# Performance work log

Hardware: AMD Instinct MI355X
Metric: run time of the kernel (lower is better)

## Reference

```python
import jax, jax.numpy as jnp
import numpy as np

B, T, D, R = 4, 2048, 512, 1024
N_INNER, N_B = 9, 2          # inner pool bins, boundary pool bins (roipool_size='2_9')
RATIO = 1.0 / 5.0            # boundary extension ratio passed to BRoI1DPool
NB = N_B + N_INNER + N_B     # 13 total bins: [start bins | inner bins | end bins]


def _bin_centers(a, b, n):
    # a, b: (B, R) -> (B, R, n) centers of n equal bins covering [a, b]
    i = (jnp.arange(n, dtype=a.dtype) + 0.5) / n
    return a[..., None] + i * (b - a)[..., None]


def broi1d_pool(feats, rois):
    # Boundary ROI 1D pooling: feats (B, T, D), rois (B, R, 2) -> (B, R, D, NB).
    # Each bin samples its center position via linear interpolation along T.
    s, e = rois[..., 0], rois[..., 1]
    ext = RATIO * (e - s)
    pos = jnp.concatenate([
        _bin_centers(s - ext, s + ext, N_B),
        _bin_centers(s, e, N_INNER),
        _bin_centers(e - ext, e + ext, N_B)], axis=-1)          # (B, R, NB)
    pos = jnp.clip(pos, 0.0, T - 1)
    lo = jnp.floor(pos).astype(jnp.int32)
    hi = jnp.minimum(lo + 1, T - 1)
    w = (pos - lo.astype(pos.dtype))[..., None]

    def gather(idx):
        g = jnp.take_along_axis(feats, idx.reshape(idx.shape[0], -1)[..., None], axis=1)
        return g.reshape(idx.shape + (feats.shape[-1],))          # (B, R, NB, D)

    vals = (1.0 - w) * gather(lo) + w * gather(hi)
    return vals.transpose(0, 1, 3, 2)                              # (B, R, D, NB)


def setup_inputs():
    key = jax.random.key(0)
    ks = jax.random.split(key, 10)
    features = jax.random.normal(ks[0], (B, T, D), jnp.float32)

    def make_rois(k):
        k1, k2 = jax.random.split(k)
        s = jax.random.uniform(k1, (B, R), jnp.float32, 0.0, T - 300.0)
        L = 16.0 + jax.random.uniform(k2, (B, R), jnp.float32) * 256.0
        return jnp.stack([s, s + L], axis=-1)

    rois = make_rois(ks[1])
    start_rois = make_rois(ks[2])
    end_rois = make_rois(ks[3])
    rois_mask = jnp.ones((B, R), jnp.float32)
    rois_pos_emb = jax.random.normal(ks[4], (B, R, D), jnp.float32)

    d_left = (N_B + N_INNER // 2 + 1) * D
    W_left = jax.random.normal(ks[5], (D, d_left), jnp.float32) / np.sqrt(d_left).astype(np.float32)
    b_left = jnp.zeros((D,), jnp.float32)
    W_inner = jax.random.normal(ks[6], (D, N_INNER * D), jnp.float32) / np.sqrt(N_INNER * D).astype(np.float32)
    b_inner = jnp.zeros((D,), jnp.float32)
    W_roi = jax.random.normal(ks[7], (D, 2 * D), jnp.float32) / np.sqrt(2 * D).astype(np.float32)
    b_roi = jnp.zeros((D,), jnp.float32)
    return {"features": features, "start_rois": start_rois, "end_rois": end_rois,
            "rois": rois, "rois_mask": rois_mask, "rois_pos_emb": rois_pos_emb,
            "W_left": W_left, "b_left": b_left, "W_inner": W_inner, "b_inner": b_inner,
            "W_roi": W_roi, "b_roi": b_roi}


def reference(features, start_rois, end_rois, rois, rois_mask, rois_pos_emb,
              W_left, b_left, W_inner, b_inner, W_roi, b_roi):
    pooled = broi1d_pool(features, rois)          # (B, R, D, NB)
    mb, r = pooled.shape[:2]

    def fc(x, W, b):
        # Linear + Dropout(eval=identity) + SELU
        return jax.nn.selu(x @ W.T + b)

    left = fc(pooled[:, :, :, 0:N_INNER // 2 + N_B + 1].reshape(mb, r, -1), W_left, b_left)
    inner = fc(pooled[:, :, :, N_B:N_INNER + N_B].reshape(mb, r, -1), W_inner, b_inner)
    # NOTE: the original code reuses left_fc for the right branch (right_fc is dead).
    right = fc(pooled[:, :, :, N_INNER // 2 + N_B:N_INNER + 2 * N_B].reshape(mb, r, -1), W_left, b_left)
    return fc(jnp.concatenate([right - left, inner], axis=2), W_roi, b_roi)  # (B, R, D)
```

## Files before the change

kernel.cpp:

```cpp
#include <hip/hip_runtime.h>
#include <hip/hip_bf16.h>
#include <cstdint>
#include <cmath>

#define BB 4
#define TT 2048
#define DD 512
#define RR 1024
#define MM (BB*RR)
#define NBINS 13
#define LDXP (NBINS*DD)

typedef __bf16 bf16;
typedef bf16 bf16x8 __attribute__((ext_vector_type(8)));
typedef bf16 bf16x2 __attribute__((ext_vector_type(2)));
typedef float f32x4 __attribute__((ext_vector_type(4)));

__device__ __forceinline__ float selu_f(float x) {
    const float sc = 1.0507009873554805f;
    const float aa = 1.6732632423543772f;
    return x > 0.0f ? sc * x : sc * aa * (expf(x) - 1.0f);
}

__device__ __forceinline__ void gload_lds16(const bf16* g, bf16* l) {
    __builtin_amdgcn_global_load_lds(
        (const __attribute__((address_space(1))) void*)g,
        (__attribute__((address_space(3))) void*)l, 16, 0, 0);
}

template<int N>
__device__ __forceinline__ void wait_vm() {
    if constexpr (N == 0)      asm volatile("s_waitcnt vmcnt(0)" ::: "memory");
    else if constexpr (N == 6) asm volatile("s_waitcnt vmcnt(6)" ::: "memory");
    else if constexpr (N == 8) asm volatile("s_waitcnt vmcnt(8)" ::: "memory");
}

template<int ROWS>
__device__ __forceinline__ void stage_tile64(const bf16* __restrict__ src, int lda,
                                             bf16* tile, int tid) {
#pragma unroll
    for (int it = 0; it < ROWS / 32; ++it) {
        int idx = it * 256 + tid;
        int row = idx >> 3;
        int col = ((idx & 7) ^ (row & 7)) * 8;
        bf16* wavebase = tile + (idx & ~63) * 8;
        gload_lds16(src + (size_t)row * lda + col, wavebase);
    }
}

__device__ __forceinline__ bf16x8 frd64(const bf16* tile, int row, int s) {
    int p = s ^ (row & 7);
    return *(const bf16x8*)(tile + row * 64 + p * 8);
}

template<int NB_, int KT>
__device__ __forceinline__ void w_row_body(const float* __restrict__ Wsrc,
                                           bf16* __restrict__ Wdst,
                                           float* ld, int n, int tid) {
    const float* src = Wsrc + (size_t)n * KT;
    for (int i = tid; i < KT; i += 256) ld[i] = src[i];
    __syncthreads();
    bf16* dst = Wdst + (size_t)n * KT;
    for (int i = tid; i < KT; i += 256) {
        int bin = i >> 9, d = i & 511;
        dst[i] = (bf16)ld[d * NB_ + bin];
    }
}

__device__ __forceinline__ void pool_body(const float* __restrict__ feats,
                                          const float* __restrict__ rois,
                                          bf16* __restrict__ Xp, int m, int tid) {
    int b = m >> 10;
    float s = rois[2 * m];
    float e = rois[2 * m + 1];
    float ext = 0.2f * (e - s);
    int d0 = tid * 2;
    bf16* orow = Xp + (size_t)m * LDXP + d0;
    const float* fb = feats + (size_t)b * TT * DD + d0;
#pragma unroll
    for (int j = 0; j < NBINS; ++j) {
        float pos;
        if (j < 2)       pos = (s - ext) + ((float)j + 0.5f) * ext;
        else if (j < 11) pos = s + (((float)(j - 2) + 0.5f) * (1.0f / 9.0f)) * (e - s);
        else             pos = (e - ext) + ((float)(j - 11) + 0.5f) * ext;
        pos = fminf(fmaxf(pos, 0.0f), (float)(TT - 1));
        float fl = floorf(pos);
        int lo = (int)fl;
        int hi = lo + 1; if (hi > TT - 1) hi = TT - 1;
        float w = pos - fl;
        float2 vlo = *(const float2*)(fb + (size_t)lo * DD);
        float2 vhi = *(const float2*)(fb + (size_t)hi * DD);
        bf16x2 o;
        o.x = (bf16)((1.0f - w) * vlo.x + w * vhi.x);
        o.y = (bf16)((1.0f - w) * vlo.y + w * vhi.y);
        *(bf16x2*)(orow + j * DD) = o;
    }
}

__global__ __launch_bounds__(256) void prep_all(
    const float* __restrict__ feats, const float* __restrict__ rois,
    const float* __restrict__ W_left, const float* __restrict__ W_inner,
    const float* __restrict__ W_roi,
    bf16* __restrict__ Xp, bf16* __restrict__ Wl, bf16* __restrict__ Wi,
    bf16* __restrict__ Wr)
{
    __shared__ float ld[4608];
    int bid = blockIdx.x, tid = threadIdx.x;
    if (bid < 4096) {
        pool_body(feats, rois, Xp, bid, tid);
    } else if (bid < 4608) {
        w_row_body<7, 3584>(W_left, Wl, ld, bid - 4096, tid);
    } else if (bid < 5120) {
        w_row_body<9, 4608>(W_inner, Wi, ld, bid - 4608, tid);
    } else {
        int i0 = (bid - 5120) * 1024 + tid * 4;
        float4 v = *(const float4*)(W_roi + i0);
        bf16* d = Wr + i0;
        d[0] = (bf16)v.x; d[1] = (bf16)v.y; d[2] = (bf16)v.z; d[3] = (bf16)v.w;
    }
}


template<int K, bool OUT_BF16>
__device__ __forceinline__ void gemm_single_body(
    const bf16* __restrict__ A, int lda,
    const bf16* __restrict__ Bw, const float* __restrict__ bias,
    void* __restrict__ Out, int ldo, int ocol0,
    bf16* sm, int m0, int n0)
{
    int tid = threadIdx.x, lane = tid & 63, w = tid >> 6;
    int wr = w >> 1, wc = w & 1;
    const bf16* Ab = A + (size_t)m0 * lda;
    const bf16* Bb = Bw + (size_t)n0 * K;
    int frow = lane & 15, sl = lane >> 4;
    f32x4 acc[2][4] = {};
    bf16 *A0 = sm,         *B0 = sm + 4096;
    bf16 *A1 = sm + 12288, *B1 = sm + 12288 + 4096;

    auto stage = [&](bf16* as, bf16* bs, int t) {
        stage_tile64<64>(Ab + t * 64, lda, as, tid);
        stage_tile64<128>(Bb + t * 64, K, bs, tid);
    };
    auto compute = [&](const bf16* as, const bf16* bs) {
#pragma unroll
        for (int ks = 0; ks < 2; ++ks) {
            bf16x8 af[2], bfr[4];
#pragma unroll
            for (int mf = 0; mf < 2; ++mf) af[mf] = frd64(as, wr * 32 + mf * 16 + frow, ks * 4 + sl);
#pragma unroll
            for (int nf = 0; nf < 4; ++nf) bfr[nf] = frd64(bs, wc * 64 + nf * 16 + frow, ks * 4 + sl);
            __builtin_amdgcn_s_setprio(1);
#pragma unroll
            for (int mf = 0; mf < 2; ++mf)
#pragma unroll
                for (int nf = 0; nf < 4; ++nf)
                    acc[mf][nf] = __builtin_amdgcn_mfma_f32_16x16x32_bf16(af[mf], bfr[nf], acc[mf][nf], 0, 0, 0);
            __builtin_amdgcn_s_setprio(0);
        }
    };

    constexpr int NT = K / 64;
    stage(A0, B0, 0);
    stage(A1, B1, 1);
    for (int t = 0; t + 2 < NT; ++t) {
        wait_vm<6>(); __builtin_amdgcn_s_barrier();
        const bf16 *as = (t & 1) ? A1 : A0, *bs = (t & 1) ? B1 : B0;
        compute(as, bs);
        __builtin_amdgcn_s_barrier();
        stage((t & 1) ? A1 : A0, (t & 1) ? B1 : B0, t + 2);
    }
    wait_vm<6>(); __builtin_amdgcn_s_barrier();
    { const bf16 *as = (NT & 1) ? A1 : A0, *bs = (NT & 1) ? B1 : B0; compute(as, bs); }
    wait_vm<0>(); __builtin_amdgcn_s_barrier();
    { const bf16 *as = (NT & 1) ? A0 : A1, *bs = (NT & 1) ? B0 : B1; compute(as, bs); }

    int crow = (lane >> 4) * 4;
    int ccol = lane & 15;
#pragma unroll
    for (int mf = 0; mf < 2; ++mf) {
#pragma unroll
        for (int nf = 0; nf < 4; ++nf) {
            int col = n0 + wc * 64 + nf * 16 + ccol;
            float bv = bias[col];
#pragma unroll
            for (int r2 = 0; r2 < 4; ++r2) {
                int row = m0 + wr * 32 + mf * 16 + crow + r2;
                float v = selu_f(acc[mf][nf][r2] + bv);
                if constexpr (OUT_BF16)
                    ((bf16*)Out)[(size_t)row * ldo + ocol0 + col] = (bf16)v;
                else
                    ((float*)Out)[(size_t)row * ldo + ocol0 + col] = v;
            }
        }
    }
}

template<int K>
__device__ __forceinline__ void gemm_dual_body(
    const bf16* __restrict__ Xp, const bf16* __restrict__ Wl,
    const float* __restrict__ bias, bf16* __restrict__ Y,
    bf16* sm, int m0, int n0)
{
    int tid = threadIdx.x, lane = tid & 63, w = tid >> 6;
    int wr = w >> 1, wc = w & 1;
    const bf16* AL = Xp + (size_t)m0 * LDXP;
    const bf16* AR = AL + 3072;
    const bf16* Bb = Wl + (size_t)n0 * K;
    int frow = lane & 15, sl = lane >> 4;
    f32x4 accL[2][4] = {}, accR[2][4] = {};
    bf16 *L0 = sm,         *R0 = sm + 4096,         *B0 = sm + 8192;
    bf16 *L1 = sm + 16384, *R1 = sm + 16384 + 4096, *B1 = sm + 16384 + 8192;

    auto stage = [&](bf16* ls, bf16* rs, bf16* bs, int t) {
        stage_tile64<64>(AL + t * 64, LDXP, ls, tid);
        stage_tile64<64>(AR + t * 64, LDXP, rs, tid);
        stage_tile64<128>(Bb + t * 64, K, bs, tid);
    };
    auto compute = [&](const bf16* ls, const bf16* rs, const bf16* bs) {
#pragma unroll
        for (int ks = 0; ks < 2; ++ks) {
            bf16x8 afL[2], afR[2], bfr[4];
#pragma unroll
            for (int mf = 0; mf < 2; ++mf) {
                afL[mf] = frd64(ls, wr * 32 + mf * 16 + frow, ks * 4 + sl);
                afR[mf] = frd64(rs, wr * 32 + mf * 16 + frow, ks * 4 + sl);
            }
#pragma unroll
            for (int nf = 0; nf < 4; ++nf) bfr[nf] = frd64(bs, wc * 64 + nf * 16 + frow, ks * 4 + sl);
            __builtin_amdgcn_s_setprio(1);
#pragma unroll
            for (int mf = 0; mf < 2; ++mf)
#pragma unroll
                for (int nf = 0; nf < 4; ++nf) {
                    accL[mf][nf] = __builtin_amdgcn_mfma_f32_16x16x32_bf16(afL[mf], bfr[nf], accL[mf][nf], 0, 0, 0);
                    accR[mf][nf] = __builtin_amdgcn_mfma_f32_16x16x32_bf16(afR[mf], bfr[nf], accR[mf][nf], 0, 0, 0);
                }
            __builtin_amdgcn_s_setprio(0);
        }
    };

    constexpr int NT = K / 64;
    stage(L0, R0, B0, 0);
    stage(L1, R1, B1, 1);
    for (int t = 0; t + 2 < NT; ++t) {
        wait_vm<8>(); __builtin_amdgcn_s_barrier();
        const bf16 *ls = (t & 1) ? L1 : L0, *rs = (t & 1) ? R1 : R0, *bs = (t & 1) ? B1 : B0;
        compute(ls, rs, bs);
        __builtin_amdgcn_s_barrier();
        stage((t & 1) ? L1 : L0, (t & 1) ? R1 : R0, (t & 1) ? B1 : B0, t + 2);
    }
    wait_vm<8>(); __builtin_amdgcn_s_barrier();
    { const bf16 *ls = (NT & 1) ? L1 : L0, *rs = (NT & 1) ? R1 : R0, *bs = (NT & 1) ? B1 : B0;
      compute(ls, rs, bs); }
    wait_vm<0>(); __builtin_amdgcn_s_barrier();
    { const bf16 *ls = (NT & 1) ? L0 : L1, *rs = (NT & 1) ? R0 : R1, *bs = (NT & 1) ? B0 : B1;
      compute(ls, rs, bs); }

    int crow = (lane >> 4) * 4;
    int ccol = lane & 15;
#pragma unroll
    for (int mf = 0; mf < 2; ++mf) {
#pragma unroll
        for (int nf = 0; nf < 4; ++nf) {
            int col = n0 + wc * 64 + nf * 16 + ccol;
            float bv = bias[col];
#pragma unroll
            for (int r2 = 0; r2 < 4; ++r2) {
                int row = m0 + wr * 32 + mf * 16 + crow + r2;
                float vL = selu_f(accL[mf][nf][r2] + bv);
                float vR = selu_f(accR[mf][nf][r2] + bv);
                Y[(size_t)row * 1024 + col] = (bf16)(vR - vL);
            }
        }
    }
}

__global__ __launch_bounds__(256) void wide_gemm(
    const bf16* __restrict__ Xp, const bf16* __restrict__ Wl,
    const float* __restrict__ bl, const bf16* __restrict__ Wi,
    const float* __restrict__ bi, bf16* __restrict__ Y)
{
    __shared__ bf16 sm[32768];
    int bid = blockIdx.x;
    if (bid < 256) {
        gemm_dual_body<3584>(Xp, Wl, bl, Y, sm, (bid & 63) * 64, (bid >> 6) * 128);
    } else {
        int b2 = bid - 256;
        gemm_single_body<4608, true>(Xp + 1024, LDXP, Wi, bi, (void*)Y, 1024, 512,
                                     sm, (b2 & 63) * 64, (b2 >> 6) * 128);
    }
}

__global__ __launch_bounds__(256) void final_gemm(
    const bf16* __restrict__ Y, const bf16* __restrict__ Wr,
    const float* __restrict__ br, float* __restrict__ out)
{
    __shared__ bf16 sm[24576];
    int bid = blockIdx.x;
    gemm_single_body<1024, false>(Y, 1024, Wr, br, (void*)out, 512, 0,
                                  sm, (bid & 63) * 64, (bid >> 6) * 128);
}

extern "C" void kernel_launch(void* const* d_in, const int* in_sizes, int n_in,
                              void* d_out, int out_size, void* d_ws, size_t ws_size,
                              hipStream_t stream) {
    const float* feats   = (const float*)d_in[0];
    const float* rois    = (const float*)d_in[3];
    const float* W_left  = (const float*)d_in[6];
    const float* b_left  = (const float*)d_in[7];
    const float* W_inner = (const float*)d_in[8];
    const float* b_inner = (const float*)d_in[9];
    const float* W_roi   = (const float*)d_in[10];
    const float* b_roi   = (const float*)d_in[11];
    float* out = (float*)d_out;

    bf16* wsb = (bf16*)d_ws;
    constexpr size_t XP_ELEMS = (size_t)MM * LDXP;
    constexpr size_t WL_ELEMS = (size_t)512 * 3584;
    constexpr size_t WI_ELEMS = (size_t)512 * 4608;
    constexpr size_t WR_ELEMS = (size_t)512 * 1024;
    bf16* Xp = wsb;
    bf16* Wl = Xp + XP_ELEMS;
    bf16* Wi = Wl + WL_ELEMS;
    bf16* Wr = Wi + WI_ELEMS;
    bf16* Y  = Wr + WR_ELEMS;

    prep_all<<<5632, 256, 0, stream>>>(feats, rois, W_left, W_inner, W_roi,
                                       Xp, Wl, Wi, Wr);
    wide_gemm<<<512, 256, 0, stream>>>(Xp, Wl, b_left, Wi, b_inner, Y);
    final_gemm<<<256, 256, 0, stream>>>(Y, Wr, b_roi, out);
}
```

Before: 111.7 us.

## Issue next tile's global loads before MFMAs by reading fragments into registers first

```diff
diff --git a/kernel.cpp b/kernel.cpp
--- a/kernel.cpp
+++ b/kernel.cpp
@@ -141,38 +141,40 @@
         stage_tile64<64>(Ab + t * 64, lda, as, tid);
         stage_tile64<128>(Bb + t * 64, K, bs, tid);
     };
-    auto compute = [&](const bf16* as, const bf16* bs) {
+    auto step_body = [&](bf16* as, bf16* bs, int t, bool dostage) {
+        __builtin_amdgcn_s_barrier();
+        bf16x8 af[2][2], bfr[2][4];
 #pragma unroll
         for (int ks = 0; ks < 2; ++ks) {
-            bf16x8 af[2], bfr[4];
-#pragma unroll
-            for (int mf = 0; mf < 2; ++mf) af[mf] = frd64(as, wr * 32 + mf * 16 + frow, ks * 4 + sl);
-#pragma unroll
-            for (int nf = 0; nf < 4; ++nf) bfr[nf] = frd64(bs, wc * 64 + nf * 16 + frow, ks * 4 + sl);
-            __builtin_amdgcn_s_setprio(1);
+#pragma unroll
+            for (int mf = 0; mf < 2; ++mf) af[ks][mf] = frd64(as, wr * 32 + mf * 16 + frow, ks * 4 + sl);
+#pragma unroll
+            for (int nf = 0; nf < 4; ++nf) bfr[ks][nf] = frd64(bs, wc * 64 + nf * 16 + frow, ks * 4 + sl);
+        }
+        asm volatile("s_waitcnt lgkmcnt(0)" ::: "memory");
+        __builtin_amdgcn_sched_barrier(0);
+        __builtin_amdgcn_s_barrier();
+        if (dostage) stage(as, bs, t + 2);
+        __builtin_amdgcn_s_setprio(1);
+#pragma unroll
+        for (int ks = 0; ks < 2; ++ks)
 #pragma unroll
             for (int mf = 0; mf < 2; ++mf)
 #pragma unroll
                 for (int nf = 0; nf < 4; ++nf)
-                    acc[mf][nf] = __builtin_amdgcn_mfma_f32_16x16x32_bf16(af[mf], bfr[nf], acc[mf][nf], 0, 0, 0);
-            __builtin_amdgcn_s_setprio(0);
-        }
+                    acc[mf][nf] = __builtin_amdgcn_mfma_f32_16x16x32_bf16(af[ks][mf], bfr[ks][nf], acc[mf][nf], 0, 0, 0);
+        __builtin_amdgcn_s_setprio(0);
     };
 
     constexpr int NT = K / 64;
     stage(A0, B0, 0);
     stage(A1, B1, 1);
-    for (int t = 0; t + 2 < NT; ++t) {
-        wait_vm<6>(); __builtin_amdgcn_s_barrier();
-        const bf16 *as = (t & 1) ? A1 : A0, *bs = (t & 1) ? B1 : B0;
-        compute(as, bs);
-        __builtin_amdgcn_s_barrier();
-        stage((t & 1) ? A1 : A0, (t & 1) ? B1 : B0, t + 2);
-    }
-    wait_vm<6>(); __builtin_amdgcn_s_barrier();
-    { const bf16 *as = (NT & 1) ? A1 : A0, *bs = (NT & 1) ? B1 : B0; compute(as, bs); }
-    wait_vm<0>(); __builtin_amdgcn_s_barrier();
-    { const bf16 *as = (NT & 1) ? A0 : A1, *bs = (NT & 1) ? B0 : B1; compute(as, bs); }
+    for (int t = 0; t + 2 < NT; t += 2) {
+        wait_vm<6>(); step_body(A0, B0, t, true);
+        wait_vm<6>(); step_body(A1, B1, t + 1, true);
+    }
+    wait_vm<6>(); step_body(A0, B0, NT - 2, false);
+    wait_vm<0>(); step_body(A1, B1, NT - 1, false);
 
     int crow = (lane >> 4) * 4;
     int ccol = lane & 15;
@@ -216,45 +218,45 @@
         stage_tile64<64>(AR + t * 64, LDXP, rs, tid);
         stage_tile64<128>(Bb + t * 64, K, bs, tid);
     };
-    auto compute = [&](const bf16* ls, const bf16* rs, const bf16* bs) {
+    auto step_body = [&](bf16* ls, bf16* rs, bf16* bs, int t, bool dostage) {
+        __builtin_amdgcn_s_barrier();
+        bf16x8 afL[2][2], afR[2][2], bfr[2][4];
 #pragma unroll
         for (int ks = 0; ks < 2; ++ks) {
-            bf16x8 afL[2], afR[2], bfr[4];
 #pragma unroll
             for (int mf = 0; mf < 2; ++mf) {
-                afL[mf] = frd64(ls, wr * 32 + mf * 16 + frow, ks * 4 + sl);
-                afR[mf] = frd64(rs, wr * 32 + mf * 16 + frow, ks * 4 + sl);
+                afL[ks][mf] = frd64(ls, wr * 32 + mf * 16 + frow, ks * 4 + sl);
+                afR[ks][mf] = frd64(rs, wr * 32 + mf * 16 + frow, ks * 4 + sl);
             }
 #pragma unroll
-            for (int nf = 0; nf < 4; ++nf) bfr[nf] = frd64(bs, wc * 64 + nf * 16 + frow, ks * 4 + sl);
-            __builtin_amdgcn_s_setprio(1);
+            for (int nf = 0; nf < 4; ++nf) bfr[ks][nf] = frd64(bs, wc * 64 + nf * 16 + frow, ks * 4 + sl);
+        }
+        asm volatile("s_waitcnt lgkmcnt(0)" ::: "memory");
+        __builtin_amdgcn_sched_barrier(0);
+        __builtin_amdgcn_s_barrier();
+        if (dostage) stage(ls, rs, bs, t + 2);
+        __builtin_amdgcn_s_setprio(1);
+#pragma unroll
+        for (int ks = 0; ks < 2; ++ks)
 #pragma unroll
             for (int mf = 0; mf < 2; ++mf)
 #pragma unroll
                 for (int nf = 0; nf < 4; ++nf) {
-                    accL[mf][nf] = __builtin_amdgcn_mfma_f32_16x16x32_bf16(afL[mf], bfr[nf], accL[mf][nf], 0, 0, 0);
-                    accR[mf][nf] = __builtin_amdgcn_mfma_f32_16x16x32_bf16(afR[mf], bfr[nf], accR[mf][nf], 0, 0, 0);
+                    accL[mf][nf] = __builtin_amdgcn_mfma_f32_16x16x32_bf16(afL[ks][mf], bfr[ks][nf], accL[mf][nf], 0, 0, 0);
+                    accR[mf][nf] = __builtin_amdgcn_mfma_f32_16x16x32_bf16(afR[ks][mf], bfr[ks][nf], accR[mf][nf], 0, 0, 0);
                 }
-            __builtin_amdgcn_s_setprio(0);
-        }
+        __builtin_amdgcn_s_setprio(0);
     };
 
     constexpr int NT = K / 64;
     stage(L0, R0, B0, 0);
     stage(L1, R1, B1, 1);
-    for (int t = 0; t + 2 < NT; ++t) {
-        wait_vm<8>(); __builtin_amdgcn_s_barrier();
-        const bf16 *ls = (t & 1) ? L1 : L0, *rs = (t & 1) ? R1 : R0, *bs = (t & 1) ? B1 : B0;
-        compute(ls, rs, bs);
-        __builtin_amdgcn_s_barrier();
-        stage((t & 1) ? L1 : L0, (t & 1) ? R1 : R0, (t & 1) ? B1 : B0, t + 2);
-    }
-    wait_vm<8>(); __builtin_amdgcn_s_barrier();
-    { const bf16 *ls = (NT & 1) ? L1 : L0, *rs = (NT & 1) ? R1 : R0, *bs = (NT & 1) ? B1 : B0;
-      compute(ls, rs, bs); }
-    wait_vm<0>(); __builtin_amdgcn_s_barrier();
-    { const bf16 *ls = (NT & 1) ? L0 : L1, *rs = (NT & 1) ? R0 : R1, *bs = (NT & 1) ? B0 : B1;
-      compute(ls, rs, bs); }
+    for (int t = 0; t + 2 < NT; t += 2) {
+        wait_vm<8>(); step_body(L0, R0, B0, t, true);
+        wait_vm<8>(); step_body(L1, R1, B1, t + 1, true);
+    }
+    wait_vm<8>(); step_body(L0, R0, B0, NT - 2, false);
+    wait_vm<0>(); step_body(L1, R1, B1, NT - 1, false);
 
     int crow = (lane >> 4) * 4;
     int ccol = lane & 15;
```

After: 104.0 us. 6.9% less time.

## Use 128x128 tiles with 512 threads and half-K staged pipeline in GEMMs

Applied to the files above, without the earlier changes.

```diff
diff --git a/kernel.cpp b/kernel.cpp
--- a/kernel.cpp
+++ b/kernel.cpp
@@ -13,7 +13,6 @@
 
 typedef __bf16 bf16;
 typedef bf16 bf16x8 __attribute__((ext_vector_type(8)));
-typedef bf16 bf16x2 __attribute__((ext_vector_type(2)));
 typedef float f32x4 __attribute__((ext_vector_type(4)));
 
 __device__ __forceinline__ float selu_f(float x) {
@@ -31,26 +30,31 @@
 template<int N>
 __device__ __forceinline__ void wait_vm() {
     if constexpr (N == 0)      asm volatile("s_waitcnt vmcnt(0)" ::: "memory");
-    else if constexpr (N == 6) asm volatile("s_waitcnt vmcnt(6)" ::: "memory");
-    else if constexpr (N == 8) asm volatile("s_waitcnt vmcnt(8)" ::: "memory");
-}
-
-template<int ROWS>
-__device__ __forceinline__ void stage_tile64(const bf16* __restrict__ src, int lda,
-                                             bf16* tile, int tid) {
-#pragma unroll
-    for (int it = 0; it < ROWS / 32; ++it) {
-        int idx = it * 256 + tid;
-        int row = idx >> 3;
-        int col = ((idx & 7) ^ (row & 7)) * 8;
-        bf16* wavebase = tile + (idx & ~63) * 8;
+    else if constexpr (N == 2) asm volatile("s_waitcnt vmcnt(2)" ::: "memory");
+    else if constexpr (N == 3) asm volatile("s_waitcnt vmcnt(3)" ::: "memory");
+}
+
+__device__ __forceinline__ void lgkm_fence() {
+    asm volatile("s_waitcnt lgkmcnt(0)" ::: "memory");
+    __builtin_amdgcn_sched_barrier(0);
+}
+
+template<int ROWS, int NTHR>
+__device__ __forceinline__ void stage_half(const bf16* __restrict__ src, int lda,
+                                           bf16* dst, int tid) {
+#pragma unroll
+    for (int it = 0; it < (ROWS * 4) / NTHR; ++it) {
+        int idx = it * NTHR + tid;
+        int row = idx >> 2;
+        int col = ((idx & 3) ^ ((row >> 1) & 3)) * 8;
+        bf16* wavebase = dst + (idx & ~63) * 8;
         gload_lds16(src + (size_t)row * lda + col, wavebase);
     }
 }
 
-__device__ __forceinline__ bf16x8 frd64(const bf16* tile, int row, int s) {
-    int p = s ^ (row & 7);
-    return *(const bf16x8*)(tile + row * 64 + p * 8);
+__device__ __forceinline__ bf16x8 frd32(const bf16* half, int row, int sl) {
+    int p = sl ^ ((row >> 1) & 3);
+    return *(const bf16x8*)(half + row * 32 + p * 8);
 }
 
 template<int NB_, int KT>
@@ -74,11 +78,14 @@
     float s = rois[2 * m];
     float e = rois[2 * m + 1];
     float ext = 0.2f * (e - s);
-    int d0 = tid * 2;
-    bf16* orow = Xp + (size_t)m * LDXP + d0;
-    const float* fb = feats + (size_t)b * TT * DD + d0;
-#pragma unroll
-    for (int j = 0; j < NBINS; ++j) {
+    int dd = (tid & 63) * 8;
+    int j0 = tid >> 6;
+    const float* fb = feats + (size_t)b * TT * DD + dd;
+    bf16* orow = Xp + (size_t)m * LDXP + dd;
+#pragma unroll
+    for (int jj = 0; jj < 4; ++jj) {
+        int j = j0 + jj * 4;
+        if (j >= NBINS) break;
         float pos;
         if (j < 2)       pos = (s - ext) + ((float)j + 0.5f) * ext;
         else if (j < 11) pos = s + (((float)(j - 2) + 0.5f) * (1.0f / 9.0f)) * (e - s);
@@ -88,12 +95,22 @@
         int lo = (int)fl;
         int hi = lo + 1; if (hi > TT - 1) hi = TT - 1;
         float w = pos - fl;
-        float2 vlo = *(const float2*)(fb + (size_t)lo * DD);
-        float2 vhi = *(const float2*)(fb + (size_t)hi * DD);
-        bf16x2 o;
-        o.x = (bf16)((1.0f - w) * vlo.x + w * vhi.x);
-        o.y = (bf16)((1.0f - w) * vlo.y + w * vhi.y);
-        *(bf16x2*)(orow + j * DD) = o;
+        const float* rlo = fb + (size_t)lo * DD;
+        const float* rhi = fb + (size_t)hi * DD;
+        float4 l0 = *(const float4*)(rlo);
+        float4 l1 = *(const float4*)(rlo + 4);
+        float4 h0 = *(const float4*)(rhi);
+        float4 h1 = *(const float4*)(rhi + 4);
+        bf16x8 o;
+        o[0] = (bf16)((1.0f - w) * l0.x + w * h0.x);
+        o[1] = (bf16)((1.0f - w) * l0.y + w * h0.y);
+        o[2] = (bf16)((1.0f - w) * l0.z + w * h0.z);
+        o[3] = (bf16)((1.0f - w) * l0.w + w * h0.w);
+        o[4] = (bf16)((1.0f - w) * l1.x + w * h1.x);
+        o[5] = (bf16)((1.0f - w) * l1.y + w * h1.y);
+        o[6] = (bf16)((1.0f - w) * l1.z + w * h1.z);
+        o[7] = (bf16)((1.0f - w) * l1.w + w * h1.w);
+        *(bf16x8*)(orow + j * DD) = o;
     }
 }
 
@@ -134,45 +151,41 @@
     const bf16* Bb = Bw + (size_t)n0 * K;
     int frow = lane & 15, sl = lane >> 4;
     f32x4 acc[2][4] = {};
-    bf16 *A0 = sm,         *B0 = sm + 4096;
-    bf16 *A1 = sm + 12288, *B1 = sm + 12288 + 4096;
-
-    auto stage = [&](bf16* as, bf16* bs, int t) {
-        stage_tile64<64>(Ab + t * 64, lda, as, tid);
-        stage_tile64<128>(Bb + t * 64, K, bs, tid);
+
+    auto stageH = [&](int t, int h) {
+        stage_half<128, 512>(Ab + t * 64 + h * 32, lda, sm + h * 4096, tid);
+        stage_half<128, 512>(Bb + t * 64 + h * 32, K, sm + 8192 + h * 4096, tid);
     };
-    auto compute = [&](const bf16* as, const bf16* bs) {
-#pragma unroll
-        for (int ks = 0; ks < 2; ++ks) {
-            bf16x8 af[2], bfr[4];
-#pragma unroll
-            for (int mf = 0; mf < 2; ++mf) af[mf] = frd64(as, wr * 32 + mf * 16 + frow, ks * 4 + sl);
-#pragma unroll
-            for (int nf = 0; nf < 4; ++nf) bfr[nf] = frd64(bs, wc * 64 + nf * 16 + frow, ks * 4 + sl);
-            __builtin_amdgcn_s_setprio(1);
-#pragma unroll
-            for (int mf = 0; mf < 2; ++mf)
-#pragma unroll
-                for (int nf = 0; nf < 4; ++nf)
-                    acc[mf][nf] = __builtin_amdgcn_mfma_f32_16x16x32_bf16(af[mf], bfr[nf], acc[mf][nf], 0, 0, 0);
-            __builtin_amdgcn_s_setprio(0);
-        }
+    auto phase = [&](int t, int h, bool dostage, bool last) {
+        if (last) wait_vm<0>(); else wait_vm<2>();
+        __builtin_amdgcn_s_barrier();
+        bf16x8 af[2], bfr[4];
+#pragma unroll
+        for (int mf = 0; mf < 2; ++mf)
+            af[mf] = frd32(sm + h * 4096, wr * 32 + mf * 16 + frow, sl);
+#pragma unroll
+        for (int nf = 0; nf < 4; ++nf)
+            bfr[nf] = frd32(sm + 8192 + h * 4096, wc * 64 + nf * 16 + frow, sl);
+        lgkm_fence();
+        __builtin_amdgcn_s_barrier();
+        if (dostage) stageH(t + 1, h);
+        __builtin_amdgcn_sched_barrier(0);
+        __builtin_amdgcn_s_setprio(1);
+#pragma unroll
+        for (int mf = 0; mf < 2; ++mf)
+#pragma unroll
+            for (int nf = 0; nf < 4; ++nf)
+                acc[mf][nf] = __builtin_amdgcn_mfma_f32_16x16x32_bf16(af[mf], bfr[nf], acc[mf][nf], 0, 0, 0);
+        __builtin_amdgcn_s_setprio(0);
     };
 
     constexpr int NT = K / 64;
-    stage(A0, B0, 0);
-    stage(A1, B1, 1);
-    for (int t = 0; t + 2 < NT; ++t) {
-        wait_vm<6>(); __builtin_amdgcn_s_barrier();
-        const bf16 *as = (t & 1) ? A1 : A0, *bs = (t & 1) ? B1 : B0;
-        compute(as, bs);
-        __builtin_amdgcn_s_barrier();
-        stage((t & 1) ? A1 : A0, (t & 1) ? B1 : B0, t + 2);
-    }
-    wait_vm<6>(); __builtin_amdgcn_s_barrier();
-    { const bf16 *as = (NT & 1) ? A1 : A0, *bs = (NT & 1) ? B1 : B0; compute(as, bs); }
-    wait_vm<0>(); __builtin_amdgcn_s_barrier();
-    { const bf16 *as = (NT & 1) ? A0 : A1, *bs = (NT & 1) ? B0 : B1; compute(as, bs); }
+    stageH(0, 0); stageH(0, 1);
+    for (int t = 0; t < NT; ++t) {
+        bool more = (t + 1 < NT);
+        phase(t, 0, more, false);
+        phase(t, 1, more, !more);
+    }
 
     int crow = (lane >> 4) * 4;
     int ccol = lane & 15;
@@ -208,53 +221,46 @@
     const bf16* Bb = Wl + (size_t)n0 * K;
     int frow = lane & 15, sl = lane >> 4;
     f32x4 accL[2][4] = {}, accR[2][4] = {};
-    bf16 *L0 = sm,         *R0 = sm + 4096,         *B0 = sm + 8192;
-    bf16 *L1 = sm + 16384, *R1 = sm + 16384 + 4096, *B1 = sm + 16384 + 8192;
-
-    auto stage = [&](bf16* ls, bf16* rs, bf16* bs, int t) {
-        stage_tile64<64>(AL + t * 64, LDXP, ls, tid);
-        stage_tile64<64>(AR + t * 64, LDXP, rs, tid);
-        stage_tile64<128>(Bb + t * 64, K, bs, tid);
+
+    auto stageH = [&](int t, int h) {
+        stage_half<128, 512>(AL + t * 64 + h * 32, LDXP, sm + h * 4096, tid);
+        stage_half<128, 512>(AR + t * 64 + h * 32, LDXP, sm + 8192 + h * 4096, tid);
+        stage_half<128, 512>(Bb + t * 64 + h * 32, K, sm + 16384 + h * 4096, tid);
     };
-    auto compute = [&](const bf16* ls, const bf16* rs, const bf16* bs) {
-#pragma unroll
-        for (int ks = 0; ks < 2; ++ks) {
-            bf16x8 afL[2], afR[2], bfr[4];
-#pragma unroll
-            for (int mf = 0; mf < 2; ++mf) {
-                afL[mf] = frd64(ls, wr * 32 + mf * 16 + frow, ks * 4 + sl);
-                afR[mf] = frd64(rs, wr * 32 + mf * 16 + frow, ks * 4 + sl);
+    auto phase = [&](int t, int h, bool dostage, bool last) {
+        if (last) wait_vm<0>(); else wait_vm<3>();
+        __builtin_amdgcn_s_barrier();
+        bf16x8 afL[2], afR[2], bfr[4];
+#pragma unroll
+        for (int mf = 0; mf < 2; ++mf) {
+            afL[mf] = frd32(sm + h * 4096, wr * 32 + mf * 16 + frow, sl);
+            afR[mf] = frd32(sm + 8192 + h * 4096, wr * 32 + mf * 16 + frow, sl);
+        }
+#pragma unroll
+        for (int nf = 0; nf < 4; ++nf)
+            bfr[nf] = frd32(sm + 16384 + h * 4096, wc * 64 + nf * 16 + frow, sl);
+        lgkm_fence();
+        __builtin_amdgcn_s_barrier();
+        if (dostage) stageH(t + 1, h);
+        __builtin_amdgcn_sched_barrier(0);
+        __builtin_amdgcn_s_setprio(1);
+#pragma unroll
+        for (int mf = 0; mf < 2; ++mf)
+#pragma unroll
+            for (int nf = 0; nf < 4; ++nf) {
+                accL[mf][nf] = __builtin_amdgcn_mfma_f32_16x16x32_bf16(afL[mf], bfr[nf], accL[mf][nf], 0, 0, 0);
+                accR[mf][nf] = __builtin_amdgcn_mfma_f32_16x16x32_bf16(afR[mf], bfr[nf], accR[mf][nf], 0, 0, 0);
             }
-#pragma unroll
-            for (int nf = 0; nf < 4; ++nf) bfr[nf] = frd64(bs, wc * 64 + nf * 16 + frow, ks * 4 + sl);
-            __builtin_amdgcn_s_setprio(1);
-#pragma unroll
-            for (int mf = 0; mf < 2; ++mf)
-#pragma unroll
-                for (int nf = 0; nf < 4; ++nf) {
-                    accL[mf][nf] = __builtin_amdgcn_mfma_f32_16x16x32_bf16(afL[mf], bfr[nf], accL[mf][nf], 0, 0, 0);
-                    accR[mf][nf] = __builtin_amdgcn_mfma_f32_16x16x32_bf16(afR[mf], bfr[nf], accR[mf][nf], 0, 0, 0);
-                }
-            __builtin_amdgcn_s_setprio(0);
-        }
+        __builtin_amdgcn_s_setprio(0);
     };
 
     constexpr int NT = K / 64;
-    stage(L0, R0, B0, 0);
-    stage(L1, R1, B1, 1);
-    for (int t = 0; t + 2 < NT; ++t) {
-        wait_vm<8>(); __builtin_amdgcn_s_barrier();
-        const bf16 *ls = (t & 1) ? L1 : L0, *rs = (t & 1) ? R1 : R0, *bs = (t & 1) ? B1 : B0;
-        compute(ls, rs, bs);
-        __builtin_amdgcn_s_barrier();
-        stage((t & 1) ? L1 : L0, (t & 1) ? R1 : R0, (t & 1) ? B1 : B0, t + 2);
-    }
-    wait_vm<8>(); __builtin_amdgcn_s_barrier();
-    { const bf16 *ls = (NT & 1) ? L1 : L0, *rs = (NT & 1) ? R1 : R0, *bs = (NT & 1) ? B1 : B0;
-      compute(ls, rs, bs); }
-    wait_vm<0>(); __builtin_amdgcn_s_barrier();
-    { const bf16 *ls = (NT & 1) ? L0 : L1, *rs = (NT & 1) ? R0 : R1, *bs = (NT & 1) ? B0 : B1;
-      compute(ls, rs, bs); }
+    stageH(0, 0); stageH(0, 1);
+    for (int t = 0; t < NT; ++t) {
+        bool more = (t + 1 < NT);
+        phase(t, 0, more, false);
+        phase(t, 1, more, !more);
+    }
 
     int crow = (lane >> 4) * 4;
     int ccol = lane & 15;
@@ -275,30 +281,30 @@
     }
 }
 
-__global__ __launch_bounds__(256) void wide_gemm(
+__global__ __launch_bounds__(512) void wide_gemm(
     const bf16* __restrict__ Xp, const bf16* __restrict__ Wl,
     const float* __restrict__ bl, const bf16* __restrict__ Wi,
     const float* __restrict__ bi, bf16* __restrict__ Y)
 {
-    __shared__ bf16 sm[32768];
+    __shared__ bf16 sm[24576];
     int bid = blockIdx.x;
-    if (bid < 256) {
-        gemm_dual_body<3584>(Xp, Wl, bl, Y, sm, (bid & 63) * 64, (bid >> 6) * 128);
+    if (bid < 128) {
+        gemm_dual_body<3584>(Xp, Wl, bl, Y, sm, (bid & 31) * 128, (bid >> 5) * 128);
     } else {
-        int b2 = bid - 256;
+        int b2 = bid - 128;
         gemm_single_body<4608, true>(Xp + 1024, LDXP, Wi, bi, (void*)Y, 1024, 512,
-                                     sm, (b2 & 63) * 64, (b2 >> 6) * 128);
-    }
-}
-
-__global__ __launch_bounds__(256) void final_gemm(
+                                     sm, (b2 & 31) * 128, (b2 >> 5) * 128);
+    }
+}
+
+__global__ __launch_bounds__(512) void final_gemm(
     const bf16* __restrict__ Y, const bf16* __restrict__ Wr,
     const float* __restrict__ br, float* __restrict__ out)
 {
-    __shared__ bf16 sm[24576];
+    __shared__ bf16 sm[16384];
     int bid = blockIdx.x;
     gemm_single_body<1024, false>(Y, 1024, Wr, br, (void*)out, 512, 0,
-                                  sm, (bid & 63) * 64, (bid >> 6) * 128);
+                                  sm, (bid & 31) * 128, (bid >> 5) * 128);
 }
 
 extern "C" void kernel_launch(void* const* d_in, const int* in_sizes, int n_in,
@@ -327,6 +333,6 @@
 
     prep_all<<<5632, 256, 0, stream>>>(feats, rois, W_left, W_inner, W_roi,
                                        Xp, Wl, Wi, Wr);
-    wide_gemm<<<512, 256, 0, stream>>>(Xp, Wl, b_left, Wi, b_inner, Y);
-    final_gemm<<<256, 256, 0, stream>>>(Y, Wr, b_roi, out);
-}
+    wide_gemm<<<256, 512, 0, stream>>>(Xp, Wl, b_left, Wi, b_inner, Y);
+    final_gemm<<<128, 512, 0, stream>>>(Y, Wr, b_roi, out);
+}
```

New measurement: 112.2 us. No clear change (+0.5%).
